# Performance work log

Hardware: AMD Instinct MI355X
Metric: run time of the kernel (lower is better)

## Reference

```python
import jax, jax.numpy as jnp
import numpy as np

N_NODES = 100000
NEG_SLOPE = 0.2


def _gatv2_layer(x, src, dst, Wl, Wr, att, Wres, b):
    # x: [N, Cin]; src/dst: [E] (edge j->i means src=j, dst=i, PyG convention)
    xl = x @ Wl                     # [N, Cout] source-side projection
    xr = x @ Wr                     # [N, Cout] target-side projection
    h = jax.nn.leaky_relu(xl[src] + xr[dst], NEG_SLOPE)   # [E, Cout]
    e = h @ att                                            # [E] attention logits
    # segment softmax over incoming edges of each dst node
    emax = jax.ops.segment_max(e, dst, num_segments=N_NODES)
    ex = jnp.exp(e - emax[dst])
    denom = jax.ops.segment_sum(ex, dst, num_segments=N_NODES)
    alpha = ex / jnp.maximum(denom[dst], 1e-16)            # [E]
    # scatter-aggregate messages (alpha * xl[src]) into dst nodes
    agg = jax.ops.segment_sum(alpha[:, None] * xl[src], dst, num_segments=N_NODES)
    # residual projection + bias (PyG GATv2Conv residual=True)
    return agg + x @ Wres + b


def setup_inputs() -> dict:
    key = jax.random.key(0)
    ks = jax.random.split(key, 12)
    C = 128
    E = 500000
    s = 1.0 / np.sqrt(C)
    inp = {
        "x": jax.random.normal(ks[0], (N_NODES, C), dtype=jnp.float32),
        "edge_index": jax.random.randint(ks[1], (2, E), 0, N_NODES, dtype=jnp.int32),
        "Wl1": jax.random.normal(ks[2], (C, C), dtype=jnp.float32) * s,
        "Wr1": jax.random.normal(ks[3], (C, C), dtype=jnp.float32) * s,
        "att1": jax.random.normal(ks[4], (C,), dtype=jnp.float32) * s,
        "Wres1": jax.random.normal(ks[5], (C, C), dtype=jnp.float32) * s,
        "b1": jnp.zeros((C,), dtype=jnp.float32),
        "Wl2": jax.random.normal(ks[6], (C, C), dtype=jnp.float32) * s,
        "Wr2": jax.random.normal(ks[7], (C, C), dtype=jnp.float32) * s,
        "att2": jax.random.normal(ks[8], (C,), dtype=jnp.float32) * s,
        "Wres2": jax.random.normal(ks[9], (C, C), dtype=jnp.float32) * s,
        "b2": jnp.zeros((C,), dtype=jnp.float32),
    }
    return inp


def reference(x, edge_index, Wl1, Wr1, att1, Wres1, b1, Wl2, Wr2, att2, Wres2, b2):
    src, dst = edge_index[0], edge_index[1]
    x = jax.nn.relu(_gatv2_layer(x, src, dst, Wl1, Wr1, att1, Wres1, b1))
    x = jax.nn.relu(_gatv2_layer(x, src, dst, Wl2, Wr2, att2, Wres2, b2))
    return x
```

## Files before the change

### kernel.cpp

```cpp
#include <hip/hip_runtime.h>
#include <math.h>

#define N_NODES 100000
#define CDIM 128
#define E_EDGES 500000
#define NEG_SLOPE 0.2f
#define SCAN_CHUNK 1024
#define SCAN_NB ((N_NODES + SCAN_CHUNK - 1) / SCAN_CHUNK)
#define NSTRIP64 ((N_NODES + 63) / 64)

typedef __attribute__((ext_vector_type(8))) short short8;
typedef __attribute__((ext_vector_type(8))) unsigned short ushort8;
typedef __attribute__((ext_vector_type(4))) unsigned short u16x4;
typedef __attribute__((ext_vector_type(4))) float f32x4;

static __device__ __forceinline__ float bf2f(unsigned short u) {
    unsigned int t = ((unsigned int)u) << 16;
    return __builtin_bit_cast(float, t);
}
static __device__ __forceinline__ unsigned short f2bf(float f) {
    unsigned int u = __builtin_bit_cast(unsigned int, f);
    unsigned int r = (u + 0x7FFFu + ((u >> 16) & 1u)) >> 16;
    return (unsigned short)r;
}
static __device__ __forceinline__ int clampi(int v, int hi) {
    return v < 0 ? 0 : (v >= hi ? hi - 1 : v);
}
static __device__ __forceinline__ float lrelu(float v) {
    return v > 0.0f ? v : NEG_SLOPE * v;
}

__global__ __launch_bounds__(256)
void pack_w_all(const float* __restrict__ W0, const float* __restrict__ W1,
                const float* __restrict__ W2, const float* __restrict__ W3,
                const float* __restrict__ W4, const float* __restrict__ W5,
                unsigned short* __restrict__ Wf) {
    const float* Wp[6] = {W0, W1, W2, W3, W4, W5};
    int mi  = blockIdx.x >> 3;
    int rem = ((blockIdx.x & 7) << 8) | threadIdx.x;
    const float* W = Wp[mi];
    int l = rem & 63, t = (rem >> 6) & 7, kk = rem >> 9;
    int m = l & 15, q = l >> 4;
    int j = t * 16 + m;
    int k0 = kk * 32 + q * 8;
    ushort8 o;
#pragma unroll
    for (int u = 0; u < 8; ++u) o[u] = f2bf(W[(k0 + u) * 128 + j]);
    *(ushort8*)(Wf + ((size_t)mi * 2048 + rem) * 8) = o;
}

template <bool XSPLIT>
__global__ __launch_bounds__(256, 3)
void projF(const void* __restrict__ Xv,
           const unsigned short* __restrict__ Wf,
           const float* __restrict__ bias,
           unsigned short* __restrict__ Aout,
           unsigned short* __restrict__ Bout,
           unsigned short* __restrict__ Rbout, int n_rows) {
    const int wave = threadIdx.x >> 6;
    const int lane = threadIdx.x & 63;
    const int m = lane & 15, q = lane >> 4;
    const int row0 = blockIdx.x * 64 + wave * 16;
    const int xrow = row0 + m;
    const int arow = xrow < n_rows ? xrow : n_rows - 1;

    short8 xh[4], xl_[4];
#pragma unroll
    for (int kk = 0; kk < 4; ++kk) {
        if (XSPLIT) {
            const float* xp = (const float*)Xv + (size_t)arow * CDIM + kk * 32 + q * 8;
            f32x4 x0 = *(const f32x4*)xp;
            f32x4 x1 = *(const f32x4*)(xp + 4);
#pragma unroll
            for (int j = 0; j < 4; ++j) {
                unsigned short h0 = f2bf(x0[j]);
                xh[kk][j] = (short)h0;
                xl_[kk][j] = (short)f2bf(x0[j] - bf2f(h0));
                unsigned short h1 = f2bf(x1[j]);
                xh[kk][4 + j] = (short)h1;
                xl_[kk][4 + j] = (short)f2bf(x1[j] - bf2f(h1));
            }
        } else {
            xh[kk] = *(const short8*)((const unsigned short*)Xv +
                                      (size_t)arow * CDIM + kk * 32 + q * 8);
        }
    }

#pragma unroll
    for (int h = 0; h < 2; ++h) {
        f32x4 acc[3][4];
#pragma unroll
        for (int mi = 0; mi < 3; ++mi)
#pragma unroll
            for (int t = 0; t < 4; ++t) acc[mi][t] = (f32x4)0.0f;

#pragma unroll
        for (int kk = 0; kk < 4; ++kk) {
            short8 w0[4], w1[4], w2[4];
#pragma unroll
            for (int tt = 0; tt < 4; ++tt) {
                const int t = h * 4 + tt;
                const size_t fo = ((size_t)(kk * 8 + t) * 64 + lane) * 8;
                w0[tt] = *(const short8*)(Wf + fo);
                w1[tt] = *(const short8*)(Wf + 16384 + fo);
                w2[tt] = *(const short8*)(Wf + 32768 + fo);
            }
            __builtin_amdgcn_sched_barrier(0);
#pragma unroll
            for (int tt = 0; tt < 4; ++tt) {
                acc[0][tt] = __builtin_amdgcn_mfma_f32_16x16x32_bf16(w0[tt], xh[kk], acc[0][tt], 0, 0, 0);
                acc[1][tt] = __builtin_amdgcn_mfma_f32_16x16x32_bf16(w1[tt], xh[kk], acc[1][tt], 0, 0, 0);
                acc[2][tt] = __builtin_amdgcn_mfma_f32_16x16x32_bf16(w2[tt], xh[kk], acc[2][tt], 0, 0, 0);
                if (XSPLIT) {
                    acc[0][tt] = __builtin_amdgcn_mfma_f32_16x16x32_bf16(w0[tt], xl_[kk], acc[0][tt], 0, 0, 0);
                    acc[1][tt] = __builtin_amdgcn_mfma_f32_16x16x32_bf16(w1[tt], xl_[kk], acc[1][tt], 0, 0, 0);
                    acc[2][tt] = __builtin_amdgcn_mfma_f32_16x16x32_bf16(w2[tt], xl_[kk], acc[2][tt], 0, 0, 0);
                }
            }
        }

        if (xrow < n_rows) {
#pragma unroll
            for (int tt = 0; tt < 4; ++tt) {
                const int t = h * 4 + tt;
                u16x4 oa, ob, orr;
                f32x4 bv = *(const f32x4*)(bias + t * 16 + q * 4);
#pragma unroll
                for (int r = 0; r < 4; ++r) {
                    oa[r] = f2bf(acc[0][tt][r]);
                    ob[r] = f2bf(acc[1][tt][r]);
                    orr[r] = f2bf(acc[2][tt][r] + bv[r]);
                }
                *(u16x4*)(Aout  + (size_t)xrow * CDIM + t * 16 + q * 4) = oa;
                *(u16x4*)(Bout  + (size_t)xrow * CDIM + t * 16 + q * 4) = ob;
                *(u16x4*)(Rbout + (size_t)xrow * CDIM + t * 16 + q * 4) = orr;
            }
        }
    }
}

__global__ __launch_bounds__(256)
void hist_dst(const int* __restrict__ dst, int* __restrict__ cnt, int n) {
    int e = blockIdx.x * 256 + threadIdx.x;
    if (e < n) atomicAdd(&cnt[clampi(dst[e], N_NODES)], 1);
}

__global__ __launch_bounds__(256)
void scan_local(const int* __restrict__ cnt, int* __restrict__ incl,
                int* __restrict__ blockSums, int n) {
    __shared__ int lds[256];
    int t = threadIdx.x;
    int base = blockIdx.x * SCAN_CHUNK + t * 4;
    int v[4], s = 0;
#pragma unroll
    for (int j = 0; j < 4; ++j) { v[j] = (base + j < n) ? cnt[base + j] : 0; s += v[j]; }
    lds[t] = s;
    __syncthreads();
    for (int off = 1; off < 256; off <<= 1) {
        int x = (t >= off) ? lds[t - off] : 0;
        __syncthreads();
        lds[t] += x;
        __syncthreads();
    }
    int run = lds[t] - s;
#pragma unroll
    for (int j = 0; j < 4; ++j) {
        run += v[j];
        if (base + j < n) incl[base + j] = run;
    }
    if (t == 255) blockSums[blockIdx.x] = lds[255];
}

__global__ __launch_bounds__(128)
void scan_sums(int* __restrict__ blockSums, int nb) {
    __shared__ int lds[128];
    int t = threadIdx.x;
    int v = (t < nb) ? blockSums[t] : 0;
    lds[t] = v;
    __syncthreads();
    for (int off = 1; off < 128; off <<= 1) {
        int x = (t >= off) ? lds[t - off] : 0;
        __syncthreads();
        lds[t] += x;
        __syncthreads();
    }
    if (t < nb) blockSums[t] = lds[t] - v;
}

__global__ __launch_bounds__(256)
void add_offsets(const int* __restrict__ incl, const int* __restrict__ blockSums,
                 const int* __restrict__ cnt, int* __restrict__ rowptr,
                 int* __restrict__ cursor, int n) {
    int i = blockIdx.x * 256 + threadIdx.x;
    if (i < n) {
        int v = incl[i] + blockSums[i / SCAN_CHUNK];
        rowptr[i + 1] = v;
        cursor[i] = v - cnt[i];
    }
    if (i == 0) rowptr[0] = 0;
}

__global__ __launch_bounds__(256)
void scatter_edges(const int* __restrict__ src, const int* __restrict__ dst,
                   int* __restrict__ cursor, int* __restrict__ esrc, int n) {
    int e = blockIdx.x * 256 + threadIdx.x;
    if (e < n) {
        int d = clampi(dst[e], N_NODES);
        int p = atomicAdd(&cursor[d], 1);
        esrc[p] = clampi(src[e], N_NODES);
    }
}

template <bool BF16OUT>
__global__ __launch_bounds__(256)
void fused_edge(const int* __restrict__ rowptr, const int* __restrict__ esrc,
                const unsigned short* __restrict__ A,
                const unsigned short* __restrict__ B,
                const float* __restrict__ att,
                const unsigned short* __restrict__ Rb, void* __restrict__ Outv,
                int n_nodes) {
    const int wave = threadIdx.x >> 6;
    const int lane = threadIdx.x & 63;
    const int g    = lane >> 4;
    const int i    = lane & 15;
    const int d    = (blockIdx.x * 4 + wave) * 4 + g;
    const bool valid = d < n_nodes;
    const int dd = valid ? d : n_nodes - 1;
    const int c0 = i * 8;

    ushort8 ub = *(const ushort8*)(B + (size_t)dd * CDIM + c0);
    float b[8], at[8];
    f32x4 at0 = *(const f32x4*)(att + c0);
    f32x4 at1 = *(const f32x4*)(att + c0 + 4);
#pragma unroll
    for (int j = 0; j < 4; ++j) {
        b[j] = bf2f(ub[j]);   b[4 + j] = bf2f(ub[4 + j]);
        at[j] = at0[j];       at[4 + j] = at1[j];
    }

    float acc[8] = {0, 0, 0, 0, 0, 0, 0, 0};
    float den = 0.0f;
    int p  = rowptr[dd];
    int p1 = valid ? rowptr[dd + 1] : p;

    for (; p < p1; ++p) {
        int s = esrc[p];
        ushort8 ua = *(const ushort8*)(A + (size_t)s * CDIM + c0);
        float a[8];
        float e = 0.0f;
#pragma unroll
        for (int j = 0; j < 8; ++j) {
            a[j] = bf2f(ua[j]);
            e += lrelu(a[j] + b[j]) * at[j];
        }
#pragma unroll
        for (int off = 8; off >= 1; off >>= 1) e += __shfl_xor(e, off, 16);
        float ee = __expf(fminf(e, 60.0f));
        den += ee;
#pragma unroll
        for (int j = 0; j < 8; ++j) acc[j] += ee * a[j];
    }

    if (valid) {
        float inv = 1.0f / fmaxf(den, 1e-16f);
        ushort8 rr = *(const ushort8*)(Rb + (size_t)d * CDIM + c0);
        float o[8];
#pragma unroll
        for (int j = 0; j < 8; ++j)
            o[j] = fmaxf(bf2f(rr[j]) + acc[j] * inv, 0.0f);
        if (BF16OUT) {
            ushort8 pk;
#pragma unroll
            for (int j = 0; j < 8; ++j) pk[j] = f2bf(o[j]);
            *(ushort8*)((unsigned short*)Outv + (size_t)d * CDIM + c0) = pk;
        } else {
            f32x4 o0, o1;
#pragma unroll
            for (int j = 0; j < 4; ++j) { o0[j] = o[j]; o1[j] = o[4 + j]; }
            float* op = (float*)Outv + (size_t)d * CDIM + c0;
            *(f32x4*)op = o0;
            *(f32x4*)(op + 4) = o1;
        }
    }
}

extern "C" void kernel_launch(void* const* d_in, const int* in_sizes, int n_in,
                              void* d_out, int out_size, void* d_ws, size_t ws_size,
                              hipStream_t stream) {
    const float* x     = (const float*)d_in[0];
    const int*   ei    = (const int*)d_in[1];
    const float* Wl1   = (const float*)d_in[2];
    const float* Wr1   = (const float*)d_in[3];
    const float* att1  = (const float*)d_in[4];
    const float* Wres1 = (const float*)d_in[5];
    const float* b1    = (const float*)d_in[6];
    const float* Wl2   = (const float*)d_in[7];
    const float* Wr2   = (const float*)d_in[8];
    const float* att2  = (const float*)d_in[9];
    const float* Wres2 = (const float*)d_in[10];
    const float* b2    = (const float*)d_in[11];

    const int* srcp = ei;
    const int* dstp = ei + E_EDGES;

    size_t off = 0;
    char* base = (char*)d_ws;
    auto carve = [&](size_t bytes) -> void* {
        void* q = base + off;
        off += (bytes + 255) & ~(size_t)255;
        return q;
    };
    unsigned short* Wf = (unsigned short*)carve((size_t)6 * 16384 * 2);
    unsigned short* A  = (unsigned short*)carve((size_t)N_NODES * CDIM * 2);
    unsigned short* B  = (unsigned short*)carve((size_t)N_NODES * CDIM * 2);
    unsigned short* X1 = (unsigned short*)carve((size_t)N_NODES * CDIM * 2);
    unsigned short* Rb = (unsigned short*)carve((size_t)N_NODES * CDIM * 2);
    int* cnt      = (int*)carve((size_t)N_NODES * 4);
    int* rowptr   = (int*)carve((size_t)(N_NODES + 1) * 4);
    int* cursor   = (int*)carve((size_t)N_NODES * 4);
    int* esrc     = (int*)carve((size_t)E_EDGES * 4);
    int* incl     = (int*)carve((size_t)N_NODES * 4);
    int* blockSums= (int*)carve((size_t)SCAN_NB * 4);
    (void)ws_size; (void)n_in; (void)in_sizes; (void)out_size;

    pack_w_all<<<48, 256, 0, stream>>>(Wl1, Wr1, Wres1, Wl2, Wr2, Wres2, Wf);

    (void)hipMemsetAsync(cnt, 0, (size_t)N_NODES * 4, stream);
    hist_dst<<<(E_EDGES + 255) / 256, 256, 0, stream>>>(dstp, cnt, E_EDGES);
    scan_local<<<SCAN_NB, 256, 0, stream>>>(cnt, incl, blockSums, N_NODES);
    scan_sums<<<1, 128, 0, stream>>>(blockSums, SCAN_NB);
    add_offsets<<<(N_NODES + 255) / 256, 256, 0, stream>>>(incl, blockSums, cnt,
                                                           rowptr, cursor, N_NODES);
    scatter_edges<<<(E_EDGES + 255) / 256, 256, 0, stream>>>(srcp, dstp, cursor,
                                                             esrc, E_EDGES);

    int egrid = (N_NODES + 15) / 16;

    projF<true ><<<NSTRIP64, 256, 0, stream>>>(x, Wf, b1, A, B, Rb, N_NODES);
    fused_edge<true ><<<egrid, 256, 0, stream>>>(rowptr, esrc, A, B, att1, Rb, X1, N_NODES);
    projF<false><<<NSTRIP64, 256, 0, stream>>>(X1, Wf + (size_t)3 * 16384, b2, A, B, Rb, N_NODES);
    fused_edge<false><<<egrid, 256, 0, stream>>>(rowptr, esrc, A, B, att2, Rb, d_out, N_NODES);
}
```

Before: 335.3 us.

## Stage projection weights through double-buffered LDS via direct global-to-LDS loads

The projection kernel now cooperatively loads each weight k-slice into a double-buffered shared-memory tile using global_load_lds, prefetching the next slice while MFMAs run on the current one. Previously every wave read the full weight fragments directly from global memory, redundantly across the four waves of a block. This adds block-wide barriers per k-step and 24KB of LDS, and lowers the launch-bounds occupancy hint from 3 to 2 blocks.

Result: faster. 315.5 us (-5.9%).

```diff
diff --git a/kernel.cpp b/kernel.cpp
--- a/kernel.cpp
+++ b/kernel.cpp
@@ -28,6 +28,12 @@
 }
 static __device__ __forceinline__ float lrelu(float v) {
     return v > 0.0f ? v : NEG_SLOPE * v;
+}
+
+static __device__ __forceinline__ void gload_lds16(const void* g, void* l) {
+    __builtin_amdgcn_global_load_lds(
+        (const __attribute__((address_space(1))) void*)g,
+        (__attribute__((address_space(3))) void*)l, 16, 0, 0);
 }
 
 __global__ __launch_bounds__(256)
@@ -50,19 +56,35 @@
 }
 
 template <bool XSPLIT>
-__global__ __launch_bounds__(256, 3)
+__global__ __launch_bounds__(256, 2)
 void projF(const void* __restrict__ Xv,
            const unsigned short* __restrict__ Wf,
            const float* __restrict__ bias,
            unsigned short* __restrict__ Aout,
            unsigned short* __restrict__ Bout,
            unsigned short* __restrict__ Rbout, int n_rows) {
+    __shared__ char wlds[2][12288];
     const int wave = threadIdx.x >> 6;
     const int lane = threadIdx.x & 63;
     const int m = lane & 15, q = lane >> 4;
     const int row0 = blockIdx.x * 64 + wave * 16;
     const int xrow = row0 + m;
     const int arow = xrow < n_rows ? xrow : n_rows - 1;
+
+    auto stage = [&](int b, int p) {
+        const int h = p >> 2, kk = p & 3;
+#pragma unroll
+        for (int c = 0; c < 3; ++c) {
+            const int s = wave * 3 + c;
+            const int mi = s >> 2;
+            const int t = h * 4 + (s & 3);
+            const char* g = (const char*)Wf + (size_t)mi * 32768 +
+                            (size_t)(kk * 8 + t) * 1024 + (size_t)lane * 16;
+            gload_lds16(g, &wlds[b][s * 1024]);
+        }
+    };
+
+    stage(0, 0);
 
     short8 xh[4], xl_[4];
 #pragma unroll
@@ -86,6 +108,8 @@
         }
     }
 
+    __syncthreads();
+
 #pragma unroll
     for (int h = 0; h < 2; ++h) {
         f32x4 acc[3][4];
@@ -96,16 +120,16 @@
 
 #pragma unroll
         for (int kk = 0; kk < 4; ++kk) {
+            const int p = h * 4 + kk;
+            if (p < 7) stage((p + 1) & 1, p + 1);
+            const char* bb = &wlds[p & 1][0];
             short8 w0[4], w1[4], w2[4];
 #pragma unroll
             for (int tt = 0; tt < 4; ++tt) {
-                const int t = h * 4 + tt;
-                const size_t fo = ((size_t)(kk * 8 + t) * 64 + lane) * 8;
-                w0[tt] = *(const short8*)(Wf + fo);
-                w1[tt] = *(const short8*)(Wf + 16384 + fo);
-                w2[tt] = *(const short8*)(Wf + 32768 + fo);
+                w0[tt] = *(const short8*)(bb + (0 * 4 + tt) * 1024 + lane * 16);
+                w1[tt] = *(const short8*)(bb + (1 * 4 + tt) * 1024 + lane * 16);
+                w2[tt] = *(const short8*)(bb + (2 * 4 + tt) * 1024 + lane * 16);
             }
-            __builtin_amdgcn_sched_barrier(0);
 #pragma unroll
             for (int tt = 0; tt < 4; ++tt) {
                 acc[0][tt] = __builtin_amdgcn_mfma_f32_16x16x32_bf16(w0[tt], xh[kk], acc[0][tt], 0, 0, 0);
@@ -117,6 +141,7 @@
                     acc[2][tt] = __builtin_amdgcn_mfma_f32_16x16x32_bf16(w2[tt], xl_[kk], acc[2][tt], 0, 0, 0);
                 }
             }
+            if (p < 7) __syncthreads();
         }
 
         if (xrow < n_rows) {
```

## Stage projection weights in LDS and use persistent blocks with atomic tile queue

Applied to the files above, without the earlier changes.

The projection kernel becomes a persistent kernel: 256 blocks of 512 threads each load all three packed weight matrices (96KB) into LDS once with global_load_lds. Waves then pull 16-row tiles from an atomic counter. Per tile, they compute all 8 output column groups from LDS-resident weights. This replaces the per-wave re-reading of weights from global/L2 memory for every strip. In exchange it adds atomic contention, large LDS use that limits occupancy, and 96 accumulator registers per lane, which may cause register pressure.

Measured after the change: 680.0 us. 103% more time.

```diff
diff --git a/kernel.cpp b/kernel.cpp
--- a/kernel.cpp
+++ b/kernel.cpp
@@ -7,7 +7,7 @@
 #define NEG_SLOPE 0.2f
 #define SCAN_CHUNK 1024
 #define SCAN_NB ((N_NODES + SCAN_CHUNK - 1) / SCAN_CHUNK)
-#define NSTRIP64 ((N_NODES + 63) / 64)
+#define NTILES ((N_NODES + 15) / 16)
 
 typedef __attribute__((ext_vector_type(8))) short short8;
 typedef __attribute__((ext_vector_type(8))) unsigned short ushort8;
@@ -28,6 +28,12 @@
 }
 static __device__ __forceinline__ float lrelu(float v) {
     return v > 0.0f ? v : NEG_SLOPE * v;
+}
+
+static __device__ __forceinline__ void gload_lds16(const void* g, void* l) {
+    __builtin_amdgcn_global_load_lds(
+        (const __attribute__((address_space(1))) void*)g,
+        (__attribute__((address_space(3))) void*)l, 16, 0, 0);
 }
 
 __global__ __launch_bounds__(256)
@@ -50,92 +56,103 @@
 }
 
 template <bool XSPLIT>
-__global__ __launch_bounds__(256, 3)
-void projF(const void* __restrict__ Xv,
+__global__ __launch_bounds__(512, 2)
+void projS(const void* __restrict__ Xv,
            const unsigned short* __restrict__ Wf,
            const float* __restrict__ bias,
            unsigned short* __restrict__ Aout,
            unsigned short* __restrict__ Bout,
-           unsigned short* __restrict__ Rbout, int n_rows) {
-    const int wave = threadIdx.x >> 6;
-    const int lane = threadIdx.x & 63;
+           unsigned short* __restrict__ Rbout,
+           int* __restrict__ tilectr, int n_tiles, int n_rows) {
+    __shared__ char wlds[98304];
+    const int tid  = threadIdx.x;
+    const int wave = tid >> 6;
+    const int lane = tid & 63;
     const int m = lane & 15, q = lane >> 4;
-    const int row0 = blockIdx.x * 64 + wave * 16;
-    const int xrow = row0 + m;
-    const int arow = xrow < n_rows ? xrow : n_rows - 1;
-
-    short8 xh[4], xl_[4];
-#pragma unroll
-    for (int kk = 0; kk < 4; ++kk) {
-        if (XSPLIT) {
-            const float* xp = (const float*)Xv + (size_t)arow * CDIM + kk * 32 + q * 8;
-            f32x4 x0 = *(const f32x4*)xp;
-            f32x4 x1 = *(const f32x4*)(xp + 4);
-#pragma unroll
-            for (int j = 0; j < 4; ++j) {
-                unsigned short h0 = f2bf(x0[j]);
-                xh[kk][j] = (short)h0;
-                xl_[kk][j] = (short)f2bf(x0[j] - bf2f(h0));
-                unsigned short h1 = f2bf(x1[j]);
-                xh[kk][4 + j] = (short)h1;
-                xl_[kk][4 + j] = (short)f2bf(x1[j] - bf2f(h1));
+
+#pragma unroll
+    for (int c = 0; c < 12; ++c) {
+        const int base = (c * 512 + wave * 64) * 16;
+        gload_lds16((const char*)Wf + base + lane * 16, wlds + base);
+    }
+    __syncthreads();
+
+    int t;
+    if (lane == 0) t = atomicAdd(tilectr, 1);
+    t = __shfl(t, 0);
+
+    while (t < n_tiles) {
+        int tn;
+        if (lane == 0) tn = atomicAdd(tilectr, 1);
+        tn = __shfl(tn, 0);
+
+        const int xrow = t * 16 + m;
+        const int arow = xrow < n_rows ? xrow : n_rows - 1;
+
+        short8 xh[4], xl_[4];
+#pragma unroll
+        for (int kk = 0; kk < 4; ++kk) {
+            if (XSPLIT) {
+                const float* xp = (const float*)Xv + (size_t)arow * CDIM + kk * 32 + q * 8;
+                f32x4 x0 = *(const f32x4*)xp;
+                f32x4 x1 = *(const f32x4*)(xp + 4);
+#pragma unroll
+                for (int j = 0; j < 4; ++j) {
+                    unsigned short h0 = f2bf(x0[j]);
+                    xh[kk][j] = (short)h0;
+                    xl_[kk][j] = (short)f2bf(x0[j] - bf2f(h0));
+                    unsigned short h1 = f2bf(x1[j]);
+                    xh[kk][4 + j] = (short)h1;
+                    xl_[kk][4 + j] = (short)f2bf(x1[j] - bf2f(h1));
+                }
+            } else {
+                xh[kk] = *(const short8*)((const unsigned short*)Xv +
+                                          (size_t)arow * CDIM + kk * 32 + q * 8);
             }
-        } else {
-            xh[kk] = *(const short8*)((const unsigned short*)Xv +
-                                      (size_t)arow * CDIM + kk * 32 + q * 8);
-        }
-    }
-
-#pragma unroll
-    for (int h = 0; h < 2; ++h) {
-        f32x4 acc[3][4];
+        }
+
+        f32x4 acc[3][8];
 #pragma unroll
         for (int mi = 0; mi < 3; ++mi)
 #pragma unroll
-            for (int t = 0; t < 4; ++t) acc[mi][t] = (f32x4)0.0f;
+            for (int tt = 0; tt < 8; ++tt) acc[mi][tt] = (f32x4)0.0f;
 
 #pragma unroll
         for (int kk = 0; kk < 4; ++kk) {
-            short8 w0[4], w1[4], w2[4];
-#pragma unroll
-            for (int tt = 0; tt < 4; ++tt) {
-                const int t = h * 4 + tt;
-                const size_t fo = ((size_t)(kk * 8 + t) * 64 + lane) * 8;
-                w0[tt] = *(const short8*)(Wf + fo);
-                w1[tt] = *(const short8*)(Wf + 16384 + fo);
-                w2[tt] = *(const short8*)(Wf + 32768 + fo);
-            }
-            __builtin_amdgcn_sched_barrier(0);
-#pragma unroll
-            for (int tt = 0; tt < 4; ++tt) {
-                acc[0][tt] = __builtin_amdgcn_mfma_f32_16x16x32_bf16(w0[tt], xh[kk], acc[0][tt], 0, 0, 0);
-                acc[1][tt] = __builtin_amdgcn_mfma_f32_16x16x32_bf16(w1[tt], xh[kk], acc[1][tt], 0, 0, 0);
-                acc[2][tt] = __builtin_amdgcn_mfma_f32_16x16x32_bf16(w2[tt], xh[kk], acc[2][tt], 0, 0, 0);
+#pragma unroll
+            for (int tt = 0; tt < 8; ++tt) {
+                const int fo = ((kk * 8 + tt) * 64 + lane) * 16;
+                short8 w0 = *(const short8*)(wlds + fo);
+                short8 w1 = *(const short8*)(wlds + 32768 + fo);
+                short8 w2 = *(const short8*)(wlds + 65536 + fo);
+                acc[0][tt] = __builtin_amdgcn_mfma_f32_16x16x32_bf16(w0, xh[kk], acc[0][tt], 0, 0, 0);
+                acc[1][tt] = __builtin_amdgcn_mfma_f32_16x16x32_bf16(w1, xh[kk], acc[1][tt], 0, 0, 0);
+                acc[2][tt] = __builtin_amdgcn_mfma_f32_16x16x32_bf16(w2, xh[kk], acc[2][tt], 0, 0, 0);
                 if (XSPLIT) {
-                    acc[0][tt] = __builtin_amdgcn_mfma_f32_16x16x32_bf16(w0[tt], xl_[kk], acc[0][tt], 0, 0, 0);
-                    acc[1][tt] = __builtin_amdgcn_mfma_f32_16x16x32_bf16(w1[tt], xl_[kk], acc[1][tt], 0, 0, 0);
-                    acc[2][tt] = __builtin_amdgcn_mfma_f32_16x16x32_bf16(w2[tt], xl_[kk], acc[2][tt], 0, 0, 0);
+                    acc[0][tt] = __builtin_amdgcn_mfma_f32_16x16x32_bf16(w0, xl_[kk], acc[0][tt], 0, 0, 0);
+                    acc[1][tt] = __builtin_amdgcn_mfma_f32_16x16x32_bf16(w1, xl_[kk], acc[1][tt], 0, 0, 0);
+                    acc[2][tt] = __builtin_amdgcn_mfma_f32_16x16x32_bf16(w2, xl_[kk], acc[2][tt], 0, 0, 0);
                 }
             }
         }
 
         if (xrow < n_rows) {
 #pragma unroll
-            for (int tt = 0; tt < 4; ++tt) {
-                const int t = h * 4 + tt;
+            for (int tt = 0; tt < 8; ++tt) {
                 u16x4 oa, ob, orr;
-                f32x4 bv = *(const f32x4*)(bias + t * 16 + q * 4);
+                f32x4 bv = *(const f32x4*)(bias + tt * 16 + q * 4);
 #pragma unroll
                 for (int r = 0; r < 4; ++r) {
                     oa[r] = f2bf(acc[0][tt][r]);
                     ob[r] = f2bf(acc[1][tt][r]);
                     orr[r] = f2bf(acc[2][tt][r] + bv[r]);
                 }
-                *(u16x4*)(Aout  + (size_t)xrow * CDIM + t * 16 + q * 4) = oa;
-                *(u16x4*)(Bout  + (size_t)xrow * CDIM + t * 16 + q * 4) = ob;
-                *(u16x4*)(Rbout + (size_t)xrow * CDIM + t * 16 + q * 4) = orr;
+                *(u16x4*)(Aout  + (size_t)xrow * CDIM + tt * 16 + q * 4) = oa;
+                *(u16x4*)(Bout  + (size_t)xrow * CDIM + tt * 16 + q * 4) = ob;
+                *(u16x4*)(Rbout + (size_t)xrow * CDIM + tt * 16 + q * 4) = orr;
             }
         }
+        t = tn;
     }
 }
 
@@ -321,11 +338,13 @@
     int* esrc     = (int*)carve((size_t)E_EDGES * 4);
     int* incl     = (int*)carve((size_t)N_NODES * 4);
     int* blockSums= (int*)carve((size_t)SCAN_NB * 4);
+    int* tilectr  = (int*)carve(2 * sizeof(int));
     (void)ws_size; (void)n_in; (void)in_sizes; (void)out_size;
 
     pack_w_all<<<48, 256, 0, stream>>>(Wl1, Wr1, Wres1, Wl2, Wr2, Wres2, Wf);
 
     (void)hipMemsetAsync(cnt, 0, (size_t)N_NODES * 4, stream);
+    (void)hipMemsetAsync(tilectr, 0, 2 * sizeof(int), stream);
     hist_dst<<<(E_EDGES + 255) / 256, 256, 0, stream>>>(dstp, cnt, E_EDGES);
     scan_local<<<SCAN_NB, 256, 0, stream>>>(cnt, incl, blockSums, N_NODES);
     scan_sums<<<1, 128, 0, stream>>>(blockSums, SCAN_NB);
@@ -336,8 +355,10 @@
 
     int egrid = (N_NODES + 15) / 16;
 
-    projF<true ><<<NSTRIP64, 256, 0, stream>>>(x, Wf, b1, A, B, Rb, N_NODES);
+    projS<true ><<<256, 512, 0, stream>>>(x, Wf, b1, A, B, Rb,
+                                          tilectr + 0, NTILES, N_NODES);
     fused_edge<true ><<<egrid, 256, 0, stream>>>(rowptr, esrc, A, B, att1, Rb, X1, N_NODES);
-    projF<false><<<NSTRIP64, 256, 0, stream>>>(X1, Wf + (size_t)3 * 16384, b2, A, B, Rb, N_NODES);
+    projS<false><<<256, 512, 0, stream>>>(X1, Wf + (size_t)3 * 16384, b2, A, B, Rb,
+                                          tilectr + 1, NTILES, N_NODES);
     fused_edge<false><<<egrid, 256, 0, stream>>>(rowptr, esrc, A, B, att2, Rb, d_out, N_NODES);
 }
```
